# Performance work log

Hardware: AMD Instinct MI355X
Metric: run time of the kernel (lower is better)

Reference implementation:

```python
import jax, jax.numpy as jnp
import numpy as np

N = 100000   # nodes
E = 1600000  # edges
DF = 256     # dim_features
H = 64       # hidden (layers=[64,64])
T = 4        # dim_target
G = 8        # graphs in batch
BN_EPS = 1e-5


def setup_inputs() -> dict:
    key = jax.random.key(0)
    ks = jax.random.split(key, 16)
    x = jax.random.normal(ks[0], (N, DF), jnp.float32)
    edge_index = jax.random.randint(ks[1], (2, E), 0, N)
    batch = jnp.sort(jax.random.randint(ks[2], (N,), 0, G))

    def lin(k, fan_in, fan_out):
        return jax.random.normal(k, (fan_in, fan_out), jnp.float32) / np.sqrt(fan_in)

    return {
        "x": x,
        "edge_index": edge_index,
        "batch": batch,
        # first_h: Linear(DF,H)+BN+ReLU
        "W_first": lin(ks[3], DF, H),
        "b_first": jnp.zeros((H,), jnp.float32),
        "bn1_g": jnp.ones((H,), jnp.float32),
        "bn1_b": jnp.zeros((H,), jnp.float32),
        # linears[0]: Linear(H,T)
        "W_lin0": lin(ks[4], H, T),
        "b_lin0": jnp.zeros((T,), jnp.float32),
        # GINConv nn: Linear(H,H)+BN+ReLU
        "W_conv": lin(ks[5], H, H),
        "b_conv": jnp.zeros((H,), jnp.float32),
        "bn2_g": jnp.ones((H,), jnp.float32),
        "bn2_b": jnp.zeros((H,), jnp.float32),
        # linears[1]: Linear(H,T)
        "W_lin1": lin(ks[6], H, T),
        "b_lin1": jnp.zeros((T,), jnp.float32),
    }


def _bn(h, gamma, beta):
    # BatchNorm1d in training mode: batch statistics over node dim
    mu = h.mean(axis=0)
    var = h.var(axis=0)
    return gamma * (h - mu) / jnp.sqrt(var + BN_EPS) + beta


def reference(x, edge_index, batch,
              W_first, b_first, bn1_g, bn1_b,
              W_lin0, b_lin0,
              W_conv, b_conv, bn2_g, bn2_b,
              W_lin1, b_lin1):
    # Layer 0: first_h = Linear+BN+ReLU
    f = jax.nn.relu(_bn(x @ W_first + b_first, bn1_g, bn1_b))  # [N,H]
    np0 = f @ W_lin0 + b_lin0                                  # [N,T]
    node_pred = np0
    wsi_pred = jax.ops.segment_max(np0, batch, num_segments=G)  # global_max_pool

    # Layer 1: GINConv (eps=0): nn(x_i + sum_{j->i} x_j)
    src, dst = edge_index[0], edge_index[1]
    agg = jax.ops.segment_sum(f[src], dst, num_segments=N)     # [N,H]
    h = f + agg
    f = jax.nn.relu(_bn(h @ W_conv + b_conv, bn2_g, bn2_b))    # [N,H]
    np1 = f @ W_lin1 + b_lin1                                  # [N,T]
    node_pred = node_pred + np1
    wsi_pred = wsi_pred + jax.ops.segment_max(np1, batch, num_segments=G)

    return wsi_pred, node_pred
```

## Files before the change

kernel.cpp:

```cpp
#include <hip/hip_runtime.h>
#include <math.h>

#define NN 100000
#define NE 1600000
#define DF 256
#define HH 64
#define TT 4
#define GG 8
#define BN_EPS 1e-5f
#define NTOT (NE + NN)

#define BROWS 512
#define NBK ((NN + BROWS - 1) / BROWS)
#define BCAP 10240
#define PCHUNK 1600
#define NPB (NE / PCHUNK)

typedef __attribute__((ext_vector_type(8))) short short8v;
typedef __attribute__((ext_vector_type(4))) float f32x4;
typedef unsigned short ushort_t;
typedef unsigned int uint_t;

__device__ __forceinline__ void atomicMaxF(float* addr, float val) {
  if (val >= 0.f) atomicMax((int*)addr, __float_as_int(val));
  else            atomicMin((unsigned int*)addr, __float_as_uint(val));
}

__device__ __forceinline__ short f2bf(float f) {
  uint_t u = __float_as_uint(f);
  u += 0x7FFFu + ((u >> 16) & 1u);
  return (short)(u >> 16);
}
__device__ __forceinline__ float bf2f(uint_t u) { return __uint_as_float(u << 16); }
__device__ __forceinline__ float bfhi(uint_t u) { return __uint_as_float(u & 0xFFFF0000u); }

__global__ void k_setup(const float* __restrict__ Wf, ushort_t* __restrict__ Wbf,
                        const float* __restrict__ Wc, ushort_t* __restrict__ Wbf2,
                        float* __restrict__ stats, float* __restrict__ maxb,
                        int* __restrict__ Bcnt) {
  int i = blockIdx.x * 256 + threadIdx.x;
  if (i < DF * HH) Wbf[i] = (ushort_t)f2bf(Wf[i]);
  else {
    int j = i - DF * HH;
    if (j < HH * HH) Wbf2[j] = (ushort_t)f2bf(Wc[j]);
  }
  if (i < 512) stats[i] = 0.f;
  if (i < 64)  maxb[i]  = -INFINITY;
  if (i < NBK) Bcnt[i]  = 0;
}

__global__ __launch_bounds__(256, 2) void k_gemm1_mfma(
    const float* __restrict__ x, const ushort_t* __restrict__ Wbf,
    const float* __restrict__ b, ushort_t* __restrict__ h1,
    float* __restrict__ stats) {
  const int lane = threadIdx.x & 63;
  const int li = lane & 15;
  const int lh = lane >> 4;
  const int gw = (blockIdx.x * 256 + (int)threadIdx.x) >> 6;
  const int nw = (gridDim.x * 256) >> 6;

  short8v bf[8][4];
#pragma unroll
  for (int s = 0; s < 8; ++s)
#pragma unroll
    for (int ct = 0; ct < 4; ++ct)
#pragma unroll
      for (int e = 0; e < 8; ++e)
        bf[s][ct][e] = (short)Wbf[(32 * s + 8 * lh + e) * HH + ct * 16 + li];

  float bias[4];
#pragma unroll
  for (int ct = 0; ct < 4; ++ct) bias[ct] = b[ct * 16 + li];

  float ps[4] = {0.f, 0.f, 0.f, 0.f}, pss[4] = {0.f, 0.f, 0.f, 0.f};

  for (int t = gw; t < NN / 16; t += nw) {
    const float* xb = x + (size_t)(t * 16 + li) * DF + 8 * lh;
    f32x4 acc[4];
#pragma unroll
    for (int ct = 0; ct < 4; ++ct) acc[ct] = (f32x4){0.f, 0.f, 0.f, 0.f};

#pragma unroll
    for (int s = 0; s < 8; ++s) {
      float4 a0 = *(const float4*)(xb + 32 * s);
      float4 a1 = *(const float4*)(xb + 32 * s + 4);
      short8v af;
      af[0] = f2bf(a0.x); af[1] = f2bf(a0.y); af[2] = f2bf(a0.z); af[3] = f2bf(a0.w);
      af[4] = f2bf(a1.x); af[5] = f2bf(a1.y); af[6] = f2bf(a1.z); af[7] = f2bf(a1.w);
#pragma unroll
      for (int ct = 0; ct < 4; ++ct)
        acc[ct] = __builtin_amdgcn_mfma_f32_16x16x32_bf16(af, bf[s][ct], acc[ct], 0, 0, 0);
    }

    ushort_t* hb = h1 + (size_t)t * 16 * HH;
#pragma unroll
    for (int ct = 0; ct < 4; ++ct) {
#pragma unroll
      for (int r = 0; r < 4; ++r) {
        float h = acc[ct][r] + bias[ct];
        hb[(lh * 4 + r) * HH + ct * 16 + li] = (ushort_t)f2bf(h);
        ps[ct] += h; pss[ct] += h * h;
      }
    }
  }

#pragma unroll
  for (int ct = 0; ct < 4; ++ct) {
    ps[ct]  += __shfl_xor(ps[ct], 16);  ps[ct]  += __shfl_xor(ps[ct], 32);
    pss[ct] += __shfl_xor(pss[ct], 16); pss[ct] += __shfl_xor(pss[ct], 32);
  }
  if (lane < 16) {
#pragma unroll
    for (int ct = 0; ct < 4; ++ct) {
      atomicAdd(&stats[ct * 16 + lane], ps[ct]);
      atomicAdd(&stats[HH + ct * 16 + lane], pss[ct]);
    }
  }
}

__global__ __launch_bounds__(256) void k_norm_gemm2(
    const ushort_t* __restrict__ h1, const float* __restrict__ stats,
    const float* __restrict__ gamma, const float* __restrict__ beta,
    const float* __restrict__ Wl0, const float* __restrict__ bl0,
    const int* __restrict__ batch, const ushort_t* __restrict__ Wbf2,
    float* __restrict__ node_pred, float* __restrict__ maxbuf,
    ushort_t* __restrict__ g) {
  __shared__ float lmax[GG * TT];
  __shared__ float abl[128];
  if (threadIdx.x < GG * TT) lmax[threadIdx.x] = -INFINITY;
  if (threadIdx.x < 64) {
    int c = threadIdx.x;
    float mu  = stats[c] * (1.f / NN);
    float var = stats[HH + c] * (1.f / NN) - mu * mu;
    float a = gamma[c] * rsqrtf(var + BN_EPS);
    abl[c] = a;
    abl[HH + c] = beta[c] - mu * a;
  }
  __syncthreads();

  const int lane = threadIdx.x & 63;
  const int li = lane & 15;
  const int lh = lane >> 4;
  const int gw = (blockIdx.x * 256 + (int)threadIdx.x) >> 6;
  const int nw = (gridDim.x * 256) >> 6;

  short8v bfr[2][4];
#pragma unroll
  for (int s = 0; s < 2; ++s)
#pragma unroll
    for (int ct = 0; ct < 4; ++ct)
#pragma unroll
      for (int e = 0; e < 8; ++e)
        bfr[s][ct][e] = (short)Wbf2[(32 * s + 8 * lh + e) * HH + ct * 16 + li];

  short8v bhd[2];
#pragma unroll
  for (int s = 0; s < 2; ++s)
#pragma unroll
    for (int e = 0; e < 8; ++e)
      bhd[s][e] = (li < TT) ? f2bf(Wl0[(32 * s + 8 * lh + e) * TT + li]) : (short)0;

  const float4 sa0 = *(const float4*)(abl + 8 * lh);
  const float4 sa1 = *(const float4*)(abl + 8 * lh + 4);
  const float4 sb0 = *(const float4*)(abl + HH + 8 * lh);
  const float4 sb1 = *(const float4*)(abl + HH + 8 * lh + 4);
  const float4 ta0 = *(const float4*)(abl + 32 + 8 * lh);
  const float4 ta1 = *(const float4*)(abl + 32 + 8 * lh + 4);
  const float4 tb0 = *(const float4*)(abl + HH + 32 + 8 * lh);
  const float4 tb1 = *(const float4*)(abl + HH + 32 + 8 * lh + 4);
  const float blv = (li < TT) ? bl0[li] : 0.f;

  for (int t = gw; t < NN / 16; t += nw) {
    const ushort_t* hb = h1 + (size_t)(t * 16 + li) * HH + 8 * lh;
    uint4 xa = *(const uint4*)(hb);
    uint4 xc = *(const uint4*)(hb + 32);

    short8v af0, af1;
    af0[0] = f2bf(fmaxf(fmaf(sa0.x, bf2f(xa.x), sb0.x), 0.f));
    af0[1] = f2bf(fmaxf(fmaf(sa0.y, bfhi(xa.x), sb0.y), 0.f));
    af0[2] = f2bf(fmaxf(fmaf(sa0.z, bf2f(xa.y), sb0.z), 0.f));
    af0[3] = f2bf(fmaxf(fmaf(sa0.w, bfhi(xa.y), sb0.w), 0.f));
    af0[4] = f2bf(fmaxf(fmaf(sa1.x, bf2f(xa.z), sb1.x), 0.f));
    af0[5] = f2bf(fmaxf(fmaf(sa1.y, bfhi(xa.z), sb1.y), 0.f));
    af0[6] = f2bf(fmaxf(fmaf(sa1.z, bf2f(xa.w), sb1.z), 0.f));
    af0[7] = f2bf(fmaxf(fmaf(sa1.w, bfhi(xa.w), sb1.w), 0.f));
    af1[0] = f2bf(fmaxf(fmaf(ta0.x, bf2f(xc.x), tb0.x), 0.f));
    af1[1] = f2bf(fmaxf(fmaf(ta0.y, bfhi(xc.x), tb0.y), 0.f));
    af1[2] = f2bf(fmaxf(fmaf(ta0.z, bf2f(xc.y), tb0.z), 0.f));
    af1[3] = f2bf(fmaxf(fmaf(ta0.w, bfhi(xc.y), tb0.w), 0.f));
    af1[4] = f2bf(fmaxf(fmaf(ta1.x, bf2f(xc.z), tb1.x), 0.f));
    af1[5] = f2bf(fmaxf(fmaf(ta1.y, bfhi(xc.z), tb1.y), 0.f));
    af1[6] = f2bf(fmaxf(fmaf(ta1.z, bf2f(xc.w), tb1.z), 0.f));
    af1[7] = f2bf(fmaxf(fmaf(ta1.w, bfhi(xc.w), tb1.w), 0.f));

    f32x4 acc[4], acch;
#pragma unroll
    for (int ct = 0; ct < 4; ++ct) {
      acc[ct] = (f32x4){0.f, 0.f, 0.f, 0.f};
      acc[ct] = __builtin_amdgcn_mfma_f32_16x16x32_bf16(af0, bfr[0][ct], acc[ct], 0, 0, 0);
      acc[ct] = __builtin_amdgcn_mfma_f32_16x16x32_bf16(af1, bfr[1][ct], acc[ct], 0, 0, 0);
    }
    acch = (f32x4){0.f, 0.f, 0.f, 0.f};
    acch = __builtin_amdgcn_mfma_f32_16x16x32_bf16(af0, bhd[0], acch, 0, 0, 0);
    acch = __builtin_amdgcn_mfma_f32_16x16x32_bf16(af1, bhd[1], acch, 0, 0, 0);

    ushort_t* gb = g + (size_t)t * 16 * HH;
#pragma unroll
    for (int ct = 0; ct < 4; ++ct)
#pragma unroll
      for (int r = 0; r < 4; ++r)
        gb[(lh * 4 + r) * HH + ct * 16 + li] = (ushort_t)f2bf(acc[ct][r]);

    if (li < TT) {
#pragma unroll
      for (int r = 0; r < 4; ++r) {
        int row = t * 16 + lh * 4 + r;
        float np = acch[r] + blv;
        atomicMaxF(&lmax[batch[row] * TT + li], np);
        node_pred[(size_t)row * TT + li] = np;
      }
    }
  }
  __syncthreads();
  if (threadIdx.x < GG * TT) atomicMaxF(&maxbuf[threadIdx.x], lmax[threadIdx.x]);
}

__global__ __launch_bounds__(256) void k_norm_np(
    const ushort_t* __restrict__ hin, const float* __restrict__ stats,
    const float* __restrict__ gamma, const float* __restrict__ beta,
    const float* __restrict__ Wlin, const float* __restrict__ blin,
    const int* __restrict__ batch, float* __restrict__ node_pred,
    float* __restrict__ maxbuf, int rpb) {
  __shared__ float lmax[GG * TT];
  __shared__ float abl[128];
  if (threadIdx.x < GG * TT) lmax[threadIdx.x] = -INFINITY;
  if (threadIdx.x < 64) {
    int c = threadIdx.x;
    float mu  = stats[c] * (1.f / NN);
    float var = stats[HH + c] * (1.f / NN) - mu * mu;
    float a = gamma[c] * rsqrtf(var + BN_EPS);
    abl[c] = a;
    abl[HH + c] = beta[c] - mu * a;
  }
  __syncthreads();

  const int lane = threadIdx.x & 63;
  const int wid  = threadIdx.x >> 6;
  const float a  = abl[lane];
  const float b2 = abl[HH + lane];
  const float4 w = ((const float4*)Wlin)[lane];
  const float4 bl = *(const float4*)blin;
  int r0 = blockIdx.x * rpb;
  int r1 = min(r0 + rpb, NN);

  for (int r = r0 + wid; r < r1; r += 4) {
    float h = bf2f(hin[(size_t)r * HH + lane]);
    float f = fmaxf(fmaf(a, h, b2), 0.f);
    float p0 = f * w.x, p1 = f * w.y, p2 = f * w.z, p3 = f * w.w;
#pragma unroll
    for (int off = 32; off; off >>= 1) {
      p0 += __shfl_xor(p0, off);
      p1 += __shfl_xor(p1, off);
      p2 += __shfl_xor(p2, off);
      p3 += __shfl_xor(p3, off);
    }
    if (lane == 0) {
      float4 np;
      np.x = p0 + bl.x; np.y = p1 + bl.y; np.z = p2 + bl.z; np.w = p3 + bl.w;
      int g = batch[r];
      atomicMaxF(&lmax[g * TT + 0], np.x);
      atomicMaxF(&lmax[g * TT + 1], np.y);
      atomicMaxF(&lmax[g * TT + 2], np.z);
      atomicMaxF(&lmax[g * TT + 3], np.w);
      float4* op = (float4*)(node_pred + (size_t)r * TT);
      float4 o = *op;
      np.x += o.x; np.y += o.y; np.z += o.z; np.w += o.w;
      *op = np;
    }
  }
  __syncthreads();
  if (threadIdx.x < GG * TT) atomicMaxF(&maxbuf[threadIdx.x], lmax[threadIdx.x]);
}

__global__ __launch_bounds__(256) void k_part(
    const int* __restrict__ ei, int* __restrict__ Bcnt,
    uint2* __restrict__ ebuf) {
  __shared__ int hist[256], start[256], cnt[256], gbase[256];
  __shared__ int ssrc[PCHUNK], sdst[PCHUNK];
  const int t = threadIdx.x;
  hist[t] = 0; cnt[t] = 0;
  __syncthreads();
  const int e0 = blockIdx.x * PCHUNK;
  for (int i = t; i < PCHUNK; i += 256)
    atomicAdd(&hist[ei[NE + e0 + i] >> 9], 1);
  __syncthreads();
  int v = hist[t];
  start[t] = v;
  __syncthreads();
  for (int off = 1; off < 256; off <<= 1) {
    int u = (t >= off) ? start[t - off] : 0;
    __syncthreads();
    start[t] += u;
    __syncthreads();
  }
  int incl = start[t];
  __syncthreads();
  start[t] = incl - v;
  if (v > 0) gbase[t] = atomicAdd(&Bcnt[t], v);
  __syncthreads();
  for (int i = t; i < PCHUNK; i += 256) {
    int src = ei[e0 + i];
    int dst = ei[NE + e0 + i];
    int b = dst >> 9;
    int p = start[b] + atomicAdd(&cnt[b], 1);
    ssrc[p] = src; sdst[p] = dst;
  }
  __syncthreads();
  for (int i = t; i < PCHUNK; i += 256) {
    int dst = sdst[i];
    int b = dst >> 9;
    uint2 pr; pr.x = (uint_t)ssrc[i]; pr.y = (uint_t)dst;
    ebuf[(size_t)b * BCAP + gbase[b] + (i - start[b])] = pr;
  }
}

__global__ void k_bscan(const int* __restrict__ Bcnt, int* __restrict__ Bbase) {
  __shared__ int s[256];
  int t = threadIdx.x;
  int v = 0;
  if (t < NBK) {
    int rows = min(BROWS, NN - t * BROWS);
    v = Bcnt[t] + rows;
  }
  s[t] = v;
  __syncthreads();
  for (int off = 1; off < 256; off <<= 1) {
    int u = (t >= off) ? s[t - off] : 0;
    __syncthreads();
    s[t] += u;
    __syncthreads();
  }
  if (t < NBK) Bbase[t] = s[t] - v;
}

__global__ __launch_bounds__(256) void k_fill2(
    const int* __restrict__ Bcnt, const int* __restrict__ Bbase,
    const uint2* __restrict__ ebuf, int* __restrict__ rowstart,
    int* __restrict__ srcl) {
  __shared__ int cnt[BROWS];
  __shared__ int ssum[256];
  const int b = blockIdx.x;
  const int r0 = b * BROWS;
  const int nrows = min(BROWS, NN - r0);
  const int ne = Bcnt[b];
  const int base = Bbase[b];
  const uint2* eb = ebuf + (size_t)b * BCAP;
  const int t = threadIdx.x;

  cnt[2 * t] = (2 * t < nrows) ? 1 : 0;
  cnt[2 * t + 1] = (2 * t + 1 < nrows) ? 1 : 0;
  __syncthreads();
  for (int j = t; j < ne; j += 256)
    atomicAdd(&cnt[(int)eb[j].y - r0], 1);
  __syncthreads();

  int a0 = cnt[2 * t], a1 = cnt[2 * t + 1];
  ssum[t] = a0 + a1;
  __syncthreads();
  for (int off = 1; off < 256; off <<= 1) {
    int u = (t >= off) ? ssum[t - off] : 0;
    __syncthreads();
    ssum[t] += u;
    __syncthreads();
  }
  int e0 = base + ssum[t] - (a0 + a1);
  int e1 = e0 + a0;
  __syncthreads();
  if (2 * t < nrows)     { rowstart[r0 + 2 * t] = e0;     srcl[e0] = r0 + 2 * t; }
  if (2 * t + 1 < nrows) { rowstart[r0 + 2 * t + 1] = e1; srcl[e1] = r0 + 2 * t + 1; }
  cnt[2 * t] = e0 + 1;
  cnt[2 * t + 1] = e1 + 1;
  __syncthreads();
  for (int j = t; j < ne; j += 256) {
    uint2 pr = eb[j];
    int p = atomicAdd(&cnt[(int)pr.y - r0], 1);
    srcl[p] = (int)pr.x;
  }
}

#define RF(x) __builtin_amdgcn_readfirstlane(x)
#define GLD(V, I) asm volatile("global_load_ushort %0, %1, %2" \
    : "=v"(V) : "v"(voff), "s"(g + (size_t)(I) * HH) : "memory")
#define WAIT16 do { asm volatile("s_waitcnt vmcnt(16)" ::: "memory"); \
    __builtin_amdgcn_sched_barrier(0); } while (0)
#define WAIT0 do { asm volatile("s_waitcnt vmcnt(0)" ::: "memory"); \
    __builtin_amdgcn_sched_barrier(0); } while (0)
#define ISSUE16(P, EB) do { \
  int j0 = RF(srcl[(EB) + 0]),  j1 = RF(srcl[(EB) + 1]); \
  int j2 = RF(srcl[(EB) + 2]),  j3 = RF(srcl[(EB) + 3]); \
  int j4 = RF(srcl[(EB) + 4]),  j5 = RF(srcl[(EB) + 5]); \
  int j6 = RF(srcl[(EB) + 6]),  j7 = RF(srcl[(EB) + 7]); \
  int j8 = RF(srcl[(EB) + 8]),  j9 = RF(srcl[(EB) + 9]); \
  int j10 = RF(srcl[(EB) + 10]), j11 = RF(srcl[(EB) + 11]); \
  int j12 = RF(srcl[(EB) + 12]), j13 = RF(srcl[(EB) + 13]); \
  int j14 = RF(srcl[(EB) + 14]), j15 = RF(srcl[(EB) + 15]); \
  GLD(P##0, j0);  GLD(P##1, j1);  GLD(P##2, j2);  GLD(P##3, j3); \
  GLD(P##4, j4);  GLD(P##5, j5);  GLD(P##6, j6);  GLD(P##7, j7); \
  GLD(P##8, j8);  GLD(P##9, j9);  GLD(P##10, j10); GLD(P##11, j11); \
  GLD(P##12, j12); GLD(P##13, j13); GLD(P##14, j14); GLD(P##15, j15); \
} while (0)
#define CJ(V, EI) do { \
  if ((EI) == nb) { \
    h2[(size_t)cur * HH + lane] = (ushort_t)f2bf(acc); ps += acc; pss += acc * acc; \
    cur++; nb = __builtin_amdgcn_readlane(rsv, cur - wra); acc = bc; \
  } \
  acc += bf2f(V); } while (0)
#define CONS16(P, EB) do { \
  CJ(P##0, (EB) + 0);  CJ(P##1, (EB) + 1);  CJ(P##2, (EB) + 2);  CJ(P##3, (EB) + 3); \
  CJ(P##4, (EB) + 4);  CJ(P##5, (EB) + 5);  CJ(P##6, (EB) + 6);  CJ(P##7, (EB) + 7); \
  CJ(P##8, (EB) + 8);  CJ(P##9, (EB) + 9);  CJ(P##10, (EB) + 10); CJ(P##11, (EB) + 11); \
  CJ(P##12, (EB) + 12); CJ(P##13, (EB) + 13); CJ(P##14, (EB) + 14); CJ(P##15, (EB) + 15); \
} while (0)

__global__ __launch_bounds__(256) void k_gather(
    const ushort_t* __restrict__ g, const int* __restrict__ rowstart,
    const int* __restrict__ srcl, const float* __restrict__ bias,
    ushort_t* __restrict__ h2, float* __restrict__ stats) {
  const int lane = threadIdx.x & 63;
  const int wid  = threadIdx.x >> 6;
  const float bc = bias[lane];
  const uint_t voff = lane * 2;
  const int wra = (blockIdx.x * 4 + wid) * 8;

  int ridx = wra + 1 + lane;
  int rsv = (ridx < NN) ? rowstart[ridx] : NTOT;

  int e    = RF(rowstart[wra]);
  int eEnd = __builtin_amdgcn_readlane(rsv, 7);
  int cur  = wra;
  int nb   = __builtin_amdgcn_readlane(rsv, 0);
  float acc = bc, ps = 0.f, pss = 0.f;

  uint_t A0, A1, A2, A3, A4, A5, A6, A7, A8, A9, A10, A11, A12, A13, A14, A15;
  uint_t B0, B1, B2, B3, B4, B5, B6, B7, B8, B9, B10, B11, B12, B13, B14, B15;

  int n = (eEnd - e) >> 4;
  if (n > 0) {
    int pend = e;
    ISSUE16(A, e); e += 16; n--;
    while (n >= 2) {
      int eb = e;
      ISSUE16(B, e); e += 16; n--;
      WAIT16; CONS16(A, pend); pend = eb;
      int ea = e;
      ISSUE16(A, e); e += 16; n--;
      WAIT16; CONS16(B, pend); pend = ea;
    }
    if (n == 1) {
      int eb = e;
      ISSUE16(B, e); e += 16;
      WAIT16; CONS16(A, pend); pend = eb;
      WAIT0;  CONS16(B, pend);
    } else {
      WAIT0;  CONS16(A, pend);
    }
  }
  for (; e < eEnd; ++e) {
    if (e == nb) {
      h2[(size_t)cur * HH + lane] = (ushort_t)f2bf(acc); ps += acc; pss += acc * acc;
      cur++; nb = __builtin_amdgcn_readlane(rsv, cur - wra); acc = bc;
    }
    int i = RF(srcl[e]);
    acc += bf2f(g[(size_t)i * HH + lane]);
  }
  h2[(size_t)cur * HH + lane] = (ushort_t)f2bf(acc); ps += acc; pss += acc * acc;

  __shared__ float sred[4][128];
  sred[wid][lane] = ps;
  sred[wid][64 + lane] = pss;
  __syncthreads();
  if (wid == 0) {
    float s0 = sred[0][lane] + sred[1][lane] + sred[2][lane] + sred[3][lane];
    float q0 = sred[0][64 + lane] + sred[1][64 + lane] + sred[2][64 + lane] + sred[3][64 + lane];
    atomicAdd(&stats[lane], s0);
    atomicAdd(&stats[HH + lane], q0);
  }
}

__global__ void k_wsi(const float* __restrict__ m0, const float* __restrict__ m1,
                      float* __restrict__ out) {
  int i = threadIdx.x;
  out[i] = m0[i] + m1[i];
}

extern "C" void kernel_launch(void* const* d_in, const int* in_sizes, int n_in,
                              void* d_out, int out_size, void* d_ws, size_t ws_size,
                              hipStream_t stream) {
  const float* x    = (const float*)d_in[0];
  const int*   ei   = (const int*)d_in[1];
  const int*   bat  = (const int*)d_in[2];
  const float* Wf   = (const float*)d_in[3];
  const float* bf   = (const float*)d_in[4];
  const float* g1   = (const float*)d_in[5];
  const float* be1  = (const float*)d_in[6];
  const float* Wl0  = (const float*)d_in[7];
  const float* bl0  = (const float*)d_in[8];
  const float* Wc   = (const float*)d_in[9];
  const float* bc   = (const float*)d_in[10];
  const float* g2   = (const float*)d_in[11];
  const float* be2  = (const float*)d_in[12];
  const float* Wl1  = (const float*)d_in[13];
  const float* bl1  = (const float*)d_in[14];

  float* out   = (float*)d_out;
  float* wsi   = out;
  float* npred = out + GG * TT;

  ushort_t* h2bf   = (ushort_t*)d_ws;
  ushort_t* h1bf   = h2bf + (size_t)NN * HH;
  ushort_t* gbf    = h1bf + (size_t)NN * HH;
  float*    stats1 = (float*)(gbf + (size_t)NN * HH);
  float*    stats2 = stats1 + 256;
  float*    maxb   = stats2 + 256;
  int*      rowstart = (int*)(maxb + 64);
  int*      Bcnt     = rowstart + NN;
  int*      Bbase    = Bcnt + 256;
  int*      srcl     = Bbase + 256;
  uint2*    ebuf     = (uint2*)(srcl + NTOT);
  ushort_t* Wbf      = (ushort_t*)(ebuf + (size_t)NBK * BCAP);
  ushort_t* Wbf2     = Wbf + DF * HH;

  k_setup<<<dim3(80), dim3(256), 0, stream>>>(Wf, Wbf, Wc, Wbf2, stats1, maxb, Bcnt);
  k_part<<<dim3(NPB), dim3(256), 0, stream>>>(ei, Bcnt, ebuf);
  k_bscan<<<dim3(1), dim3(256), 0, stream>>>(Bcnt, Bbase);
  k_fill2<<<dim3(NBK), dim3(256), 0, stream>>>(Bcnt, Bbase, ebuf, rowstart, srcl);

  k_gemm1_mfma<<<dim3(512), dim3(256), 0, stream>>>(x, Wbf, bf, h1bf, stats1);
  k_norm_gemm2<<<dim3(512), dim3(256), 0, stream>>>(
      h1bf, stats1, g1, be1, Wl0, bl0, bat, Wbf2, npred, maxb, gbf);

  k_gather<<<dim3(NN / 32), dim3(256), 0, stream>>>(
      gbf, rowstart, srcl, bc, h2bf, stats2);
  k_norm_np<<<dim3(512), dim3(256), 0, stream>>>(
      h2bf, stats2, g2, be2, Wl1, bl1, bat, npred, maxb + 32, (NN + 511) / 512);

  k_wsi<<<dim3(1), dim3(32), 0, stream>>>(maxb, maxb + 32, wsi);
}
```

Measured before the change: 295.2 us.

## Gather two bf16 features per lane, splitting wave halves across row groups

The GIN neighbor-sum gather now has each 32-lane half-wave load a full 128-byte bf16 row with dword loads, so each lane accumulates two features, and the two halves of a wave handle two different groups of 8 destination rows. This halves the number of load instructions per edge compared with per-lane ushort loads and doubles the rows each wave covers. Blocks shrink to 128 threads while the grid stays the same. Row boundaries move to LDS, and the per-feature stats are reduced with a cross-half shuffle. The cost is divergence when the two halves have different edge counts, since the shorter half issues clamped redundant loads, plus a per-edge bounds check.

```diff
diff --git a/kernel.cpp b/kernel.cpp
--- a/kernel.cpp
+++ b/kernel.cpp
@@ -19,6 +19,7 @@
 typedef __attribute__((ext_vector_type(8))) short short8v;
 typedef __attribute__((ext_vector_type(4))) float f32x4;
 typedef unsigned short ushort_t;
+typedef unsigned char uchar_t;
 typedef unsigned int uint_t;
 
 __device__ __forceinline__ void atomicMaxF(float* addr, float val) {
@@ -389,101 +390,121 @@
 }
 
 #define RF(x) __builtin_amdgcn_readfirstlane(x)
-#define GLD(V, I) asm volatile("global_load_ushort %0, %1, %2" \
-    : "=v"(V) : "v"(voff), "s"(g + (size_t)(I) * HH) : "memory")
+#define MINI(a, b) ((a) < (b) ? (a) : (b))
 #define WAIT16 do { asm volatile("s_waitcnt vmcnt(16)" ::: "memory"); \
     __builtin_amdgcn_sched_barrier(0); } while (0)
 #define WAIT0 do { asm volatile("s_waitcnt vmcnt(0)" ::: "memory"); \
     __builtin_amdgcn_sched_barrier(0); } while (0)
-#define ISSUE16(P, EB) do { \
-  int j0 = RF(srcl[(EB) + 0]),  j1 = RF(srcl[(EB) + 1]); \
-  int j2 = RF(srcl[(EB) + 2]),  j3 = RF(srcl[(EB) + 3]); \
-  int j4 = RF(srcl[(EB) + 4]),  j5 = RF(srcl[(EB) + 5]); \
-  int j6 = RF(srcl[(EB) + 6]),  j7 = RF(srcl[(EB) + 7]); \
-  int j8 = RF(srcl[(EB) + 8]),  j9 = RF(srcl[(EB) + 9]); \
-  int j10 = RF(srcl[(EB) + 10]), j11 = RF(srcl[(EB) + 11]); \
-  int j12 = RF(srcl[(EB) + 12]), j13 = RF(srcl[(EB) + 13]); \
-  int j14 = RF(srcl[(EB) + 14]), j15 = RF(srcl[(EB) + 15]); \
-  GLD(P##0, j0);  GLD(P##1, j1);  GLD(P##2, j2);  GLD(P##3, j3); \
-  GLD(P##4, j4);  GLD(P##5, j5);  GLD(P##6, j6);  GLD(P##7, j7); \
-  GLD(P##8, j8);  GLD(P##9, j9);  GLD(P##10, j10); GLD(P##11, j11); \
-  GLD(P##12, j12); GLD(P##13, j13); GLD(P##14, j14); GLD(P##15, j15); \
+#define GLD2(V, IA, IB) do { \
+  uint_t _row = (uint_t)(half ? (IB) : (IA)); \
+  const uchar_t* _p = g8 + (((size_t)_row) << 7) + boff; \
+  asm volatile("global_load_dword %0, %1, off" : "=v"(V) : "v"(_p) : "memory"); \
 } while (0)
-#define CJ(V, EI) do { \
-  if ((EI) == nb) { \
-    h2[(size_t)cur * HH + lane] = (ushort_t)f2bf(acc); ps += acc; pss += acc * acc; \
-    cur++; nb = __builtin_amdgcn_readlane(rsv, cur - wra); acc = bc; \
+#define IST(P, K, CA, CB) do { \
+  int _ia = RF(srcl[MINI((CA) + (K), eLastA)]); \
+  int _ib = RF(srcl[MINI((CB) + (K), eLastB)]); \
+  GLD2(P##K, _ia, _ib); \
+} while (0)
+#define ISSUE16P(P, CA, CB) do { \
+  IST(P, 0, CA, CB);  IST(P, 1, CA, CB);  IST(P, 2, CA, CB);  IST(P, 3, CA, CB); \
+  IST(P, 4, CA, CB);  IST(P, 5, CA, CB);  IST(P, 6, CA, CB);  IST(P, 7, CA, CB); \
+  IST(P, 8, CA, CB);  IST(P, 9, CA, CB);  IST(P, 10, CA, CB); IST(P, 11, CA, CB); \
+  IST(P, 12, CA, CB); IST(P, 13, CA, CB); IST(P, 14, CA, CB); IST(P, 15, CA, CB); \
+} while (0)
+#define FLUSHROW do { \
+  uint_t _o = ((uint_t)(ushort_t)f2bf(acc0)) | (((uint_t)(ushort_t)f2bf(acc1)) << 16); \
+  *(uint_t*)(h2 + (size_t)cur * HH + 2 * q) = _o; \
+  ps0 += acc0; ps1 += acc1; pq0 += acc0 * acc0; pq1 += acc1 * acc1; \
+  cur += 1; nb = bnd[wid][cur - wra]; acc0 = bb.x; acc1 = bb.y; \
+} while (0)
+#define CJ2(V) do { \
+  if (ec < eEnd) { \
+    if (ec == nb) { FLUSHROW; } \
+    acc0 += bf2f(V); acc1 += bfhi(V); \
   } \
-  acc += bf2f(V); } while (0)
-#define CONS16(P, EB) do { \
-  CJ(P##0, (EB) + 0);  CJ(P##1, (EB) + 1);  CJ(P##2, (EB) + 2);  CJ(P##3, (EB) + 3); \
-  CJ(P##4, (EB) + 4);  CJ(P##5, (EB) + 5);  CJ(P##6, (EB) + 6);  CJ(P##7, (EB) + 7); \
-  CJ(P##8, (EB) + 8);  CJ(P##9, (EB) + 9);  CJ(P##10, (EB) + 10); CJ(P##11, (EB) + 11); \
-  CJ(P##12, (EB) + 12); CJ(P##13, (EB) + 13); CJ(P##14, (EB) + 14); CJ(P##15, (EB) + 15); \
+  ec += 1; \
 } while (0)
-
-__global__ __launch_bounds__(256) void k_gather(
+#define CONS16P(P) do { \
+  CJ2(P##0);  CJ2(P##1);  CJ2(P##2);  CJ2(P##3); \
+  CJ2(P##4);  CJ2(P##5);  CJ2(P##6);  CJ2(P##7); \
+  CJ2(P##8);  CJ2(P##9);  CJ2(P##10); CJ2(P##11); \
+  CJ2(P##12); CJ2(P##13); CJ2(P##14); CJ2(P##15); \
+} while (0)
+
+__global__ __launch_bounds__(128) void k_gather(
     const ushort_t* __restrict__ g, const int* __restrict__ rowstart,
     const int* __restrict__ srcl, const float* __restrict__ bias,
     ushort_t* __restrict__ h2, float* __restrict__ stats) {
+  __shared__ int bnd[2][16];
+  __shared__ float sred[2][128];
+  const uchar_t* g8 = (const uchar_t*)g;
   const int lane = threadIdx.x & 63;
   const int wid  = threadIdx.x >> 6;
-  const float bc = bias[lane];
-  const uint_t voff = lane * 2;
-  const int wra = (blockIdx.x * 4 + wid) * 8;
+  const int half = lane >> 5;
+  const int q    = lane & 31;
+  const uint_t boff = (uint_t)q * 4;
+  const int wra = RF((blockIdx.x * 2 + wid) * 16);
 
   int ridx = wra + 1 + lane;
-  int rsv = (ridx < NN) ? rowstart[ridx] : NTOT;
-
-  int e    = RF(rowstart[wra]);
-  int eEnd = __builtin_amdgcn_readlane(rsv, 7);
-  int cur  = wra;
-  int nb   = __builtin_amdgcn_readlane(rsv, 0);
-  float acc = bc, ps = 0.f, pss = 0.f;
+  if (lane < 16) bnd[wid][lane] = (ridx < NN) ? rowstart[ridx] : NTOT;
+  __syncthreads();
+
+  const float2 bb = ((const float2*)bias)[q];
+  const int eA0   = RF(rowstart[wra]);
+  const int eEndA = RF(bnd[wid][7]);
+  const int eEndB = RF(bnd[wid][15]);
+  const int eB0   = eEndA;
+  const int eLastA = eEndA - 1;
+  const int eLastB = eEndB - 1;
+
+  int eEnd = half ? eEndB : eEndA;
+  int ec   = half ? eB0 : eA0;
+  int cur  = half ? wra + 8 : wra;
+  int nb   = bnd[wid][cur - wra];
+  float acc0 = bb.x, acc1 = bb.y;
+  float ps0 = 0.f, ps1 = 0.f, pq0 = 0.f, pq1 = 0.f;
 
   uint_t A0, A1, A2, A3, A4, A5, A6, A7, A8, A9, A10, A11, A12, A13, A14, A15;
   uint_t B0, B1, B2, B3, B4, B5, B6, B7, B8, B9, B10, B11, B12, B13, B14, B15;
 
-  int n = (eEnd - e) >> 4;
+  int cA = eA0, cB = eB0;
+  int nA = (eEndA - eA0 + 15) >> 4;
+  int nB = (eEndB - eB0 + 15) >> 4;
+  int n = nA > nB ? nA : nB;
+
   if (n > 0) {
-    int pend = e;
-    ISSUE16(A, e); e += 16; n--;
+    ISSUE16P(A, cA, cB); cA += 16; cB += 16; n--;
     while (n >= 2) {
-      int eb = e;
-      ISSUE16(B, e); e += 16; n--;
-      WAIT16; CONS16(A, pend); pend = eb;
-      int ea = e;
-      ISSUE16(A, e); e += 16; n--;
-      WAIT16; CONS16(B, pend); pend = ea;
+      ISSUE16P(B, cA, cB); cA += 16; cB += 16; n--;
+      WAIT16; CONS16P(A);
+      ISSUE16P(A, cA, cB); cA += 16; cB += 16; n--;
+      WAIT16; CONS16P(B);
     }
     if (n == 1) {
-      int eb = e;
-      ISSUE16(B, e); e += 16;
-      WAIT16; CONS16(A, pend); pend = eb;
-      WAIT0;  CONS16(B, pend);
+      ISSUE16P(B, cA, cB);
+      WAIT16; CONS16P(A);
+      WAIT0;  CONS16P(B);
     } else {
-      WAIT0;  CONS16(A, pend);
-    }
-  }
-  for (; e < eEnd; ++e) {
-    if (e == nb) {
-      h2[(size_t)cur * HH + lane] = (ushort_t)f2bf(acc); ps += acc; pss += acc * acc;
-      cur++; nb = __builtin_amdgcn_readlane(rsv, cur - wra); acc = bc;
-    }
-    int i = RF(srcl[e]);
-    acc += bf2f(g[(size_t)i * HH + lane]);
-  }
-  h2[(size_t)cur * HH + lane] = (ushort_t)f2bf(acc); ps += acc; pss += acc * acc;
-
-  __shared__ float sred[4][128];
-  sred[wid][lane] = ps;
-  sred[wid][64 + lane] = pss;
-  __syncthreads();
-  if (wid == 0) {
-    float s0 = sred[0][lane] + sred[1][lane] + sred[2][lane] + sred[3][lane];
-    float q0 = sred[0][64 + lane] + sred[1][64 + lane] + sred[2][64 + lane] + sred[3][64 + lane];
-    atomicAdd(&stats[lane], s0);
-    atomicAdd(&stats[HH + lane], q0);
+      WAIT0;  CONS16P(A);
+    }
+  }
+  {
+    uint_t o = ((uint_t)(ushort_t)f2bf(acc0)) | (((uint_t)(ushort_t)f2bf(acc1)) << 16);
+    *(uint_t*)(h2 + (size_t)cur * HH + 2 * q) = o;
+    ps0 += acc0; ps1 += acc1; pq0 += acc0 * acc0; pq1 += acc1 * acc1;
+  }
+
+  ps0 += __shfl_xor(ps0, 32); ps1 += __shfl_xor(ps1, 32);
+  pq0 += __shfl_xor(pq0, 32); pq1 += __shfl_xor(pq1, 32);
+  if (half == 0) {
+    sred[wid][2 * q] = ps0;      sred[wid][2 * q + 1] = ps1;
+    sred[wid][64 + 2 * q] = pq0; sred[wid][64 + 2 * q + 1] = pq1;
+  }
+  __syncthreads();
+  if (threadIdx.x < 64) {
+    int l = threadIdx.x;
+    atomicAdd(&stats[l], sred[0][l] + sred[1][l]);
+    atomicAdd(&stats[HH + l], sred[0][64 + l] + sred[1][64 + l]);
   }
 }
 
@@ -539,7 +560,7 @@
   k_norm_gemm2<<<dim3(512), dim3(256), 0, stream>>>(
       h1bf, stats1, g1, be1, Wl0, bl0, bat, Wbf2, npred, maxb, gbf);
 
-  k_gather<<<dim3(NN / 32), dim3(256), 0, stream>>>(
+  k_gather<<<dim3(NN / 32), dim3(128), 0, stream>>>(
       gbf, rowstart, srcl, bc, h2bf, stats2);
   k_norm_np<<<dim3(512), dim3(256), 0, stream>>>(
       h2bf, stats2, g2, be2, Wl1, bl1, bat, npred, maxb + 32, (NN + 511) / 512);
```

Result: slower. 308.2 us (+4.4%).
